# Kernel optimization log

Measured on AMD Instinct MI355X. Metric: run time of the kernel, lower is better.

The kernel has to match this reference:

```python
import jax, jax.numpy as jnp
import numpy as np
import math

B, L, D, H = 2, 2048, 1024, 16
DH = D // H  # d_head = 64
FACTOR = 5


def setup_inputs() -> dict:
    key = jax.random.key(0)
    ks = jax.random.split(key, 6)
    s = 0.02
    x = jax.random.normal(ks[0], (B, L, D), jnp.float32)
    Wq = jax.random.normal(ks[1], (D, D), jnp.float32) * s
    bq = jnp.zeros((D,), jnp.float32)
    Wkv = jax.random.normal(ks[2], (2 * D, D), jnp.float32) * s
    bkv = jnp.zeros((2 * D,), jnp.float32)
    Wout = jax.random.normal(ks[3], (D, D), jnp.float32) * s
    bout = jnp.zeros((D,), jnp.float32)
    U = min(FACTOR * math.ceil(math.log(L)), L)  # 40
    index_sample = jax.random.randint(ks[4], (L, U), 0, L, dtype=jnp.int32)
    return {"x": x, "Wq": Wq, "bq": bq, "Wkv": Wkv, "bkv": bkv,
            "Wout": Wout, "bout": bout, "index_sample": index_sample,
            "factor": FACTOR}


def reference(x, Wq, bq, Wkv, bkv, Wout, bout, index_sample, factor):
    b, l, d = x.shape
    h, dh = H, DH
    scale = 1.0 / math.sqrt(dh)
    u = min(factor * math.ceil(math.log(l)), l)

    # projections (torch Linear: y = x @ W.T + b)
    Q = (x @ Wq.T + bq).reshape(b, l, h, dh).transpose(0, 2, 1, 3)   # [B,H,L,dh]
    KV = x @ Wkv.T + bkv
    K, V = jnp.split(KV, 2, axis=-1)
    K = K.reshape(b, l, h, dh).transpose(0, 2, 1, 3)                  # [B,H,L,dh]
    V = V.reshape(b, l, h, dh).transpose(0, 2, 1, 3)                  # [B,H,L,dh]

    # sampled QK: per query position l, dot with U sampled keys
    K_s = K[:, :, index_sample, :]                                    # [B,H,L,U,dh]
    QK = jnp.einsum('bhld,bhlud->bhlu', Q, K_s)                       # [B,H,L,U]
    M = QK.max(axis=-1) - QK.mean(axis=-1)                            # sparsity measure
    _, top_idx = jax.lax.top_k(M, u)                                  # [B,H,u]

    # full attention only for the top-u queries
    top_q = jnp.take_along_axis(Q, top_idx[..., None], axis=2)        # [B,H,u,dh]
    scores = jnp.einsum('bhud,bhkd->bhuk', top_q, K) * scale          # [B,H,u,L]
    attn = jax.nn.softmax(scores, axis=-1)
    ctx_update = jnp.einsum('bhuk,bhkd->bhud', attn, V)               # [B,H,u,dh]

    # mean-initialized context, scatter updates at top queries
    context = jnp.broadcast_to(V.mean(axis=2, keepdims=True), (b, h, l, dh))
    bI = jnp.arange(b)[:, None, None]
    hI = jnp.arange(h)[None, :, None]
    context = context.at[bI, hI, top_idx].set(ctx_update)             # [B,H,L,dh]

    context = context.transpose(0, 2, 1, 3).reshape(b, l, d)
    return context @ Wout.T + bout
```

## Files before the change

kernel.cpp:

```cpp
#include <hip/hip_runtime.h>
#include <math.h>

#define B_ 2
#define L_ 2048
#define D_ 1024
#define H_ 16
#define DH_ 64
#define U_ 40
#define SCALE_ 0.125f

typedef __attribute__((ext_vector_type(8))) short short8v;
typedef __attribute__((ext_vector_type(4))) float f32x4;
typedef __attribute__((ext_vector_type(4))) unsigned short ushort4v;

static __device__ __forceinline__ unsigned short bf16_rne(float f) {
  unsigned int u = __float_as_uint(f);
  u += 0x7fff + ((u >> 16) & 1);
  return (unsigned short)(u >> 16);
}
static __device__ __forceinline__ float bf16_f32(unsigned short h) {
  return __uint_as_float(((unsigned int)h) << 16);
}

static __device__ __forceinline__ void gload16(const unsigned short* src,
                                               unsigned short* lds) {
  __builtin_amdgcn_global_load_lds(
      (const __attribute__((address_space(1))) void*)src,
      (__attribute__((address_space(3))) void*)lds, 16, 0, 0);
}

#define BARRIER                                  \
  do {                                           \
    asm volatile("" ::: "memory");               \
    __builtin_amdgcn_s_barrier();                \
    asm volatile("" ::: "memory");               \
  } while (0)
#define LGKM0                                          \
  do {                                                 \
    asm volatile("s_waitcnt lgkmcnt(0)" ::: "memory"); \
    __builtin_amdgcn_sched_barrier(0);                 \
  } while (0)

__global__ __launch_bounds__(256) void split_all(
    const float* __restrict__ Wq, const float* __restrict__ Wkv,
    const float* __restrict__ X, unsigned short* __restrict__ Whi,
    unsigned short* __restrict__ Wlo, unsigned short* __restrict__ Xhi,
    unsigned short* __restrict__ Xlo, float* __restrict__ vmAcc, int nW) {
  if (blockIdx.x == 0) {
    for (int z = threadIdx.x; z < B_ * D_; z += 256) vmAcc[z] = 0.f;
  }
  int i = blockIdx.x * 256 + threadIdx.x;
  const int nq_q = (D_ * D_) / 4;
  float4 v;
  unsigned short *hi, *lo;
  int off;
  if (i < nW) {
    v = (i < nq_q) ? ((const float4*)Wq)[i] : ((const float4*)Wkv)[i - nq_q];
    hi = Whi; lo = Wlo; off = i;
  } else {
    off = i - nW;
    v = ((const float4*)X)[off];
    hi = Xhi; lo = Xlo;
  }
  float vv[4] = {v.x, v.y, v.z, v.w};
  ushort4v h, l;
#pragma unroll
  for (int e = 0; e < 4; ++e) {
    unsigned short hh = bf16_rne(vv[e]);
    h[e] = hh;
    l[e] = bf16_rne(vv[e] - bf16_f32(hh));
  }
  ((ushort4v*)hi)[off] = h;
  ((ushort4v*)lo)[off] = l;
}

__global__ __launch_bounds__(512, 1) void gemm_qkv_pipe(
    const unsigned short* __restrict__ Xhi,
    const unsigned short* __restrict__ Xlo,
    const unsigned short* __restrict__ Whi,
    const unsigned short* __restrict__ Wlo,
    const float* __restrict__ bq, const float* __restrict__ bkv,
    float* __restrict__ Qo, float* __restrict__ Ko, float* __restrict__ Vo,
    float* __restrict__ vmAcc) {
  __shared__ unsigned short LDS[3][20480];
  const int tid = threadIdx.x;
  const int lane = tid & 63;
  const int wave = tid >> 6;
  const int wm = wave >> 2, wn = wave & 3;
  const int row0 = blockIdx.y * 128;
  const int col0 = blockIdx.x * 192;

  f32x4 acc[4][3] = {};

  const unsigned short* gsrc[5];
#pragma unroll
  for (int r = 0; r < 5; ++r) {
    int c = wave + 8 * r;
    const unsigned short* base;
    int rowin, isA;
    if (c < 8)       { base = Xhi; rowin = c * 16;        isA = 1; }
    else if (c < 16) { base = Xlo; rowin = (c - 8) * 16;  isA = 1; }
    else if (c < 28) { base = Whi; rowin = (c - 16) * 16; isA = 0; }
    else             { base = Wlo; rowin = (c - 28) * 16; isA = 0; }
    rowin += (lane >> 2);
    int grow = (isA ? row0 : col0) + rowin;
    int seg = (lane & 3) ^ ((rowin >> 1) & 3);
    gsrc[r] = base + (size_t)grow * D_ + seg * 8;
  }

  const int fr_r = lane & 15;
  const int hs = lane >> 4;

#define STG(r, k0s, Ls) \
  gload16(gsrc[r] + (k0s), (Ls) + (wave + 8 * (r)) * 512)

  {
    unsigned short* L0 = &LDS[0][0];
    unsigned short* L1 = &LDS[1][0];
    STG(0, 0, L0); STG(1, 0, L0); STG(2, 0, L0); STG(3, 0, L0); STG(4, 0, L0);
    STG(0, 32, L1); STG(1, 32, L1); STG(2, 32, L1); STG(3, 32, L1);
    STG(4, 32, L1);
  }
  asm volatile("s_waitcnt vmcnt(5)" ::: "memory");
  BARRIER;

  for (int ks = 0; ks < 32; ++ks) {
    unsigned short* Lc = &LDS[ks % 3][0];
    unsigned short* Ls = &LDS[(ks + 2) % 3][0];
    int k0s = (ks + 2) * 32;

    if (ks < 30) {
      STG(0, k0s, Ls); STG(1, k0s, Ls); STG(2, k0s, Ls); STG(3, k0s, Ls);
      STG(4, k0s, Ls);
    }

    short8v a_h[4], a_l[4], b_h[3], b_l[3];
#pragma unroll
    for (int mi = 0; mi < 4; ++mi) {
      int rr = wm * 64 + mi * 16 + fr_r;
      int off = rr * 32 + ((hs ^ ((rr >> 1) & 3)) << 3);
      a_h[mi] = *(const short8v*)&Lc[off];
      a_l[mi] = *(const short8v*)&Lc[4096 + off];
    }
#pragma unroll
    for (int ni = 0; ni < 3; ++ni) {
      int rc = wn * 48 + ni * 16 + fr_r;
      int off = rc * 32 + ((hs ^ ((rc >> 1) & 3)) << 3);
      b_h[ni] = *(const short8v*)&Lc[8192 + off];
      b_l[ni] = *(const short8v*)&Lc[14336 + off];
    }

#pragma unroll
    for (int mi = 0; mi < 4; ++mi)
#pragma unroll
      for (int ni = 0; ni < 3; ++ni) {
        acc[mi][ni] = __builtin_amdgcn_mfma_f32_16x16x32_bf16(
            a_h[mi], b_h[ni], acc[mi][ni], 0, 0, 0);
        acc[mi][ni] = __builtin_amdgcn_mfma_f32_16x16x32_bf16(
            a_h[mi], b_l[ni], acc[mi][ni], 0, 0, 0);
        acc[mi][ni] = __builtin_amdgcn_mfma_f32_16x16x32_bf16(
            a_l[mi], b_h[ni], acc[mi][ni], 0, 0, 0);
      }

    LGKM0;
    if (ks < 30) {
      asm volatile("s_waitcnt vmcnt(5)" ::: "memory");
    } else {
      asm volatile("s_waitcnt vmcnt(0)" ::: "memory");
    }
    BARRIER;
  }

#pragma unroll
  for (int ni = 0; ni < 3; ++ni) {
    int c = col0 + wn * 48 + ni * 16 + (lane & 15);
    int which = c >> 10;
    int jj = c & (D_ - 1);
    int h = jj >> 6, dh = jj & 63;
    float bias = (c < D_) ? bq[c] : bkv[c - D_];
    float* dst = (which == 0) ? Qo : ((which == 1) ? Ko : Vo);
#pragma unroll
    for (int mi = 0; mi < 4; ++mi) {
#pragma unroll
      for (int reg = 0; reg < 4; ++reg) {
        int r = row0 + wm * 64 + mi * 16 + ((lane >> 4) << 2) + reg;
        int b = r >> 11, l = r & (L_ - 1);
        dst[(((size_t)b * H_ + h) * L_ + l) * DH_ + dh] =
            acc[mi][ni][reg] + bias;
      }
    }
    if (which == 2) {
      float s = 0.f;
#pragma unroll
      for (int mi = 0; mi < 4; ++mi)
#pragma unroll
        for (int reg = 0; reg < 4; ++reg) s += acc[mi][ni][reg];
      s += __shfl_xor(s, 16);
      s += __shfl_xor(s, 32);
      if ((lane >> 4) == 0)
        atomicAdd(&vmAcc[(row0 >> 11) * D_ + jj], s + 64.0f * bias);
    }
  }
#undef STG
}

__global__ __launch_bounds__(256) void gemm_qkv_fallback(
    const float* __restrict__ X,
    const unsigned short* __restrict__ Whi,
    const unsigned short* __restrict__ Wlo,
    const float* __restrict__ bq, const float* __restrict__ bkv,
    float* __restrict__ Qo, float* __restrict__ Ko, float* __restrict__ Vo,
    float* __restrict__ vmAcc) {
  __shared__ unsigned short Ah[128 * 32];
  __shared__ unsigned short Al[128 * 32];
  __shared__ unsigned short Bh[128 * 32];
  __shared__ unsigned short Bl[128 * 32];
  const int tid = threadIdx.x;
  const int lane = tid & 63;
  const int wave = tid >> 6;
  const int wm = wave >> 1, wn = wave & 1;
  const int row0 = blockIdx.y * 128;
  const int col0 = blockIdx.x * 128;

  f32x4 acc[4][4] = {};

  const int grow = lane >> 2;
  const int gg = lane & 3;

  for (int k0 = 0; k0 < D_; k0 += 32) {
#pragma unroll
    for (int j = 0; j < 2; ++j) {
      int c = wave + 4 * j;
      int row = c * 16 + grow;
      int gsrc = (gg ^ ((row >> 1) & 3)) << 3;
      size_t soffB = (size_t)(col0 + row) * D_ + k0 + gsrc;
      gload16(Whi + soffB, Bh + c * 512);
      gload16(Wlo + soffB, Bl + c * 512);
    }
#pragma unroll
    for (int rep = 0; rep < 2; ++rep) {
      int task = tid + rep * 256;
      int row = task >> 2;
      int gt = task & 3;
      const float* s = X + (size_t)(row0 + row) * D_ + k0 + gt * 8;
      float4 a0 = *(const float4*)s;
      float4 a1 = *(const float4*)(s + 4);
      float av[8] = {a0.x, a0.y, a0.z, a0.w, a1.x, a1.y, a1.z, a1.w};
      short8v hseg, lseg;
#pragma unroll
      for (int e = 0; e < 8; ++e) {
        unsigned short hh = bf16_rne(av[e]);
        hseg[e] = (short)hh;
        lseg[e] = (short)bf16_rne(av[e] - bf16_f32(hh));
      }
      int dst = row * 32 + ((gt ^ ((row >> 1) & 3)) << 3);
      *(short8v*)&Ah[dst] = hseg;
      *(short8v*)&Al[dst] = lseg;
    }
    __syncthreads();

    short8v a_h[4], a_l[4], b_h[4], b_l[4];
    const int hs = lane >> 4;
#pragma unroll
    for (int mi = 0; mi < 4; ++mi) {
      int rr = wm * 64 + mi * 16 + (lane & 15);
      int off = rr * 32 + ((hs ^ ((rr >> 1) & 3)) << 3);
      a_h[mi] = *(const short8v*)&Ah[off];
      a_l[mi] = *(const short8v*)&Al[off];
    }
#pragma unroll
    for (int ni = 0; ni < 4; ++ni) {
      int rc = wn * 64 + ni * 16 + (lane & 15);
      int off = rc * 32 + ((hs ^ ((rc >> 1) & 3)) << 3);
      b_h[ni] = *(const short8v*)&Bh[off];
      b_l[ni] = *(const short8v*)&Bl[off];
    }
#pragma unroll
    for (int mi = 0; mi < 4; ++mi)
#pragma unroll
      for (int ni = 0; ni < 4; ++ni) {
        acc[mi][ni] = __builtin_amdgcn_mfma_f32_16x16x32_bf16(
            a_h[mi], b_h[ni], acc[mi][ni], 0, 0, 0);
        acc[mi][ni] = __builtin_amdgcn_mfma_f32_16x16x32_bf16(
            a_h[mi], b_l[ni], acc[mi][ni], 0, 0, 0);
        acc[mi][ni] = __builtin_amdgcn_mfma_f32_16x16x32_bf16(
            a_l[mi], b_h[ni], acc[mi][ni], 0, 0, 0);
      }
    __syncthreads();
  }

#pragma unroll
  for (int ni = 0; ni < 4; ++ni) {
    int c = col0 + wn * 64 + ni * 16 + (lane & 15);
    int which = c >> 10;
    int jj = c & (D_ - 1);
    int h = jj >> 6, dh = jj & 63;
    float bias = (c < D_) ? bq[c] : bkv[c - D_];
    float* dst = (which == 0) ? Qo : ((which == 1) ? Ko : Vo);
#pragma unroll
    for (int mi = 0; mi < 4; ++mi) {
#pragma unroll
      for (int reg = 0; reg < 4; ++reg) {
        int r = row0 + wm * 64 + mi * 16 + ((lane >> 4) << 2) + reg;
        int b = r >> 11, l = r & (L_ - 1);
        dst[(((size_t)b * H_ + h) * L_ + l) * DH_ + dh] =
            acc[mi][ni][reg] + bias;
      }
    }
    if (which == 2) {
      float s = 0.f;
#pragma unroll
      for (int mi = 0; mi < 4; ++mi)
#pragma unroll
        for (int reg = 0; reg < 4; ++reg) s += acc[mi][ni][reg];
      s += __shfl_xor(s, 16);
      s += __shfl_xor(s, 32);
      if ((lane >> 4) == 0)
        atomicAdd(&vmAcc[(row0 >> 11) * D_ + jj], s + 64.0f * bias);
    }
  }
}

__global__ __launch_bounds__(256) void sample_base(
    const float* __restrict__ Q, const float* __restrict__ Kt,
    const int* __restrict__ idx, float* __restrict__ Mv,
    const float* __restrict__ vmAcc, const float* __restrict__ Wout,
    const float* __restrict__ bout, float* __restrict__ baseOut,
    float* __restrict__ vmeanM) {
  int t = threadIdx.x;
  if (blockIdx.x < 4096) {
    int w = t >> 6, lane = t & 63;
    int subl = lane >> 4, d16 = lane & 15;
    int gl = blockIdx.x * 16 + w * 4 + subl;
    int bh = gl >> 11, l = gl & (L_ - 1);
    const float4* Kb4 = (const float4*)(Kt + (size_t)bh * L_ * DH_);
    float4 q4 = ((const float4*)(Q + (size_t)gl * DH_))[d16];
    const int* irow = idx + l * U_;
    float mx = -INFINITY, sm = 0.f;
#pragma unroll 8
    for (int u = 0; u < U_; ++u) {
      int kl = irow[u];
      float4 k4 = Kb4[kl * 16 + d16];
      float p = q4.x * k4.x + q4.y * k4.y + q4.z * k4.z + q4.w * k4.w;
      p += __shfl_xor(p, 1);
      p += __shfl_xor(p, 2);
      p += __shfl_xor(p, 4);
      p += __shfl_xor(p, 8);
      mx = fmaxf(mx, p);
      sm += p;
    }
    if (d16 == 0) Mv[gl] = mx - sm * (1.0f / U_);
  } else {
    int bid = blockIdx.x - 4096;
    int b = bid >> 4, jc = bid & 15;
    int j = jc * 64 + (t & 63);
    int isl = t >> 6;
    __shared__ float vm[D_];
    __shared__ float red[256];
    for (int i = t; i < D_; i += 256) vm[i] = vmAcc[b * D_ + i] * (1.0f / L_);
    __syncthreads();
    if (jc == 0)
      for (int i = t; i < D_; i += 256) vmeanM[b * D_ + i] = vm[i];
    float s = 0.f;
    const float* wr = Wout + (size_t)j * D_ + isl * 256;
    const float* vv = vm + isl * 256;
    for (int i = 0; i < 256; i += 4) {
      float4 w = *(const float4*)(wr + i);
      s += vv[i] * w.x + vv[i + 1] * w.y + vv[i + 2] * w.z + vv[i + 3] * w.w;
    }
    red[t] = s;
    __syncthreads();
    if (isl == 0)
      baseOut[b * D_ + j] =
          red[t] + red[t + 64] + red[t + 128] + red[t + 192] + bout[j];
  }
}

__global__ __launch_bounds__(256) void bcast_topk(
    const float* __restrict__ baseIn, float* __restrict__ out,
    const float* __restrict__ Mv, int* __restrict__ topIdx) {
  int t = threadIdx.x;
  if (blockIdx.x < 4096) {
    size_t i4 = (size_t)blockIdx.x * 256 + t;
    size_t i = i4 * 4;
    int b = (int)(i >> 21);
    int col = (int)(i & (D_ - 1));
    *(float4*)(out + i) = *(const float4*)(baseIn + b * D_ + col);
  } else {
    __shared__ float vals[L_];
    int lane = t & 63;
    int bh = blockIdx.x - 4096;
    for (int j = t; j < L_; j += 256) vals[j] = Mv[(size_t)bh * L_ + j];
    __syncthreads();
    for (int it = 0; it < U_; ++it) {
      float bv = -INFINITY;
      int bi = 0x7fffffff;
      for (int j = 0; j < 32; ++j) {
        int i = j * 64 + lane;
        float v = vals[i];
        if (v > bv) { bv = v; bi = i; }
      }
#pragma unroll
      for (int off = 32; off > 0; off >>= 1) {
        float ov = __shfl_xor(bv, off);
        int oi = __shfl_xor(bi, off);
        if (ov > bv || (ov == bv && oi < bi)) { bv = ov; bi = oi; }
      }
      if (t == 0) topIdx[bh * U_ + it] = bi;
      vals[bi] = -INFINITY;
      __syncthreads();
    }
  }
}

__global__ __launch_bounds__(256) void attn_corr(
    const float* __restrict__ Q, const float* __restrict__ Kt,
    const float* __restrict__ Vt, const int* __restrict__ topIdx,
    const float* __restrict__ vmeanM, const float* __restrict__ Wout,
    float* __restrict__ out) {
  int qc = blockIdx.x;
  int bh = blockIdx.y;
  int b = bh >> 4, h = bh & (H_ - 1);
  __shared__ float Qs[5][DH_];
  __shared__ float Sv[5][L_];
  __shared__ float part[4][5][DH_];
  __shared__ float inv[5];
  __shared__ float dv[5][DH_];
  __shared__ int lq[5];
  int t = threadIdx.x;
  int lane = t & 63, w = t >> 6;

  if (t < 80) {
    int q = t >> 4, c4 = t & 15;
    int ql = topIdx[bh * U_ + qc * 5 + q];
    *(float4*)&Qs[q][c4 * 4] =
        *(const float4*)&Q[((size_t)bh * L_ + ql) * DH_ + c4 * 4];
  }
  if (t < 5) lq[t] = topIdx[bh * U_ + qc * 5 + t];
  __syncthreads();

  const float* Kb = Kt + (size_t)bh * L_ * DH_;
  for (int kc = 0; kc < 8; ++kc) {
    int key = kc * 256 + t;
    const float* kr = Kb + (size_t)key * DH_;
    float acc[5];
#pragma unroll
    for (int q = 0; q < 5; ++q) acc[q] = 0.f;
#pragma unroll
    for (int i4 = 0; i4 < 16; ++i4) {
      float4 k4 = *(const float4*)(kr + i4 * 4);
#pragma unroll
      for (int q = 0; q < 5; ++q) {
        float4 qv = *(const float4*)&Qs[q][i4 * 4];
        acc[q] += k4.x * qv.x + k4.y * qv.y + k4.z * qv.z + k4.w * qv.w;
      }
    }
#pragma unroll
    for (int q = 0; q < 5; ++q) Sv[q][key] = acc[q] * SCALE_;
  }
  __syncthreads();

#pragma unroll
  for (int rep = 0; rep < 2; ++rep) {
    int r = (rep == 0) ? w : (w == 0 ? 4 : -1);
    if (r >= 0) {
      float mx = -INFINITY;
      for (int j = 0; j < 32; ++j) mx = fmaxf(mx, Sv[r][j * 64 + lane]);
#pragma unroll
      for (int off = 1; off < 64; off <<= 1)
        mx = fmaxf(mx, __shfl_xor(mx, off));
      float sm = 0.f;
      for (int j = 0; j < 32; ++j) {
        float e = __expf(Sv[r][j * 64 + lane] - mx);
        Sv[r][j * 64 + lane] = e;
        sm += e;
      }
#pragma unroll
      for (int off = 1; off < 64; off <<= 1) sm += __shfl_xor(sm, off);
      if (lane == 0) inv[r] = 1.0f / sm;
    }
  }
  __syncthreads();

  {
    const float* vb = Vt + ((size_t)bh * L_ + w * 512) * DH_ + lane;
    float acc[5];
#pragma unroll
    for (int q = 0; q < 5; ++q) acc[q] = 0.f;
    for (int k4 = 0; k4 < 128; ++k4) {
      float v0 = vb[(k4 * 4 + 0) * DH_];
      float v1 = vb[(k4 * 4 + 1) * DH_];
      float v2 = vb[(k4 * 4 + 2) * DH_];
      float v3 = vb[(k4 * 4 + 3) * DH_];
      int k = w * 512 + k4 * 4;
#pragma unroll
      for (int q = 0; q < 5; ++q) {
        float4 p4 = *(const float4*)&Sv[q][k];
        acc[q] += p4.x * v0 + p4.y * v1 + p4.z * v2 + p4.w * v3;
      }
    }
#pragma unroll
    for (int q = 0; q < 5; ++q) part[w][q][lane] = acc[q];
  }
  __syncthreads();

  for (int o = t; o < 5 * DH_; o += 256) {
    int q = o >> 6, dh = o & 63;
    float s = (part[0][q][dh] + part[1][q][dh]) +
              (part[2][q][dh] + part[3][q][dh]);
    dv[q][dh] = s * inv[q] - vmeanM[b * D_ + h * DH_ + dh];
  }
  __syncthreads();

  int sub = t & 3;
  int jbase = t >> 2;
#pragma unroll
  for (int jc = 0; jc < 16; ++jc) {
    int j = jc * 64 + jbase;
    const float* wr = Wout + (size_t)j * D_ + h * DH_ + sub * 16;
    float4 w0 = ((const float4*)wr)[0];
    float4 w1 = ((const float4*)wr)[1];
    float4 w2 = ((const float4*)wr)[2];
    float4 w3 = ((const float4*)wr)[3];
#pragma unroll
    for (int q = 0; q < 5; ++q) {
      const float* dq = &dv[q][sub * 16];
      float s = dq[0] * w0.x + dq[1] * w0.y + dq[2] * w0.z + dq[3] * w0.w +
                dq[4] * w1.x + dq[5] * w1.y + dq[6] * w1.z + dq[7] * w1.w +
                dq[8] * w2.x + dq[9] * w2.y + dq[10] * w2.z + dq[11] * w2.w +
                dq[12] * w3.x + dq[13] * w3.y + dq[14] * w3.z + dq[15] * w3.w;
      s += __shfl_xor(s, 1);
      s += __shfl_xor(s, 2);
      if (sub == 0)
        atomicAdd(out + ((size_t)b * L_ + lq[q]) * D_ + j, s);
    }
  }
}

extern "C" void kernel_launch(void* const* d_in, const int* in_sizes, int n_in,
                              void* d_out, int out_size, void* d_ws,
                              size_t ws_size, hipStream_t stream) {
  const float* x    = (const float*)d_in[0];
  const float* Wq   = (const float*)d_in[1];
  const float* bq   = (const float*)d_in[2];
  const float* Wkv  = (const float*)d_in[3];
  const float* bkv  = (const float*)d_in[4];
  const float* Wout = (const float*)d_in[5];
  const float* bout = (const float*)d_in[6];
  const int*   idx  = (const int*)d_in[7];
  float* out = (float*)d_out;

  float* ws = (float*)d_ws;
  const size_t NQ = (size_t)B_ * H_ * L_ * DH_;
  float* Q  = ws;
  float* Kt = Q + NQ;
  float* Vt = Kt + NQ;
  unsigned short* Whi = (unsigned short*)(Vt + NQ);
  unsigned short* Wlo = Whi + (size_t)3 * D_ * D_;
  unsigned short* Xhi = Wlo + (size_t)3 * D_ * D_;
  unsigned short* Xlo = Xhi + NQ;
  float* Mv     = Vt + NQ;
  float* vmeanM = Mv + (size_t)B_ * H_ * L_;
  float* baseB  = vmeanM + B_ * D_;
  int*   topIdx = (int*)(baseB + B_ * D_);
  float* vmAcc = out;

  const bool xsplit = ws_size >= ((size_t)76 << 20);
  const int nW = 3 * D_ * D_ / 4;
  const int nX = (int)(NQ / 4);

  if (xsplit) {
    split_all<<<dim3((nW + nX) / 256), dim3(256), 0, stream>>>(
        Wq, Wkv, x, Whi, Wlo, Xhi, Xlo, vmAcc, nW);
    gemm_qkv_pipe<<<dim3(3 * D_ / 192, B_ * L_ / 128), dim3(512), 0,
                    stream>>>(Xhi, Xlo, Whi, Wlo, bq, bkv, Q, Kt, Vt, vmAcc);
  } else {
    split_all<<<dim3(nW / 256), dim3(256), 0, stream>>>(Wq, Wkv, x, Whi, Wlo,
                                                        Xhi, Xlo, vmAcc, nW);
    gemm_qkv_fallback<<<dim3(3 * D_ / 128, B_ * L_ / 128), dim3(256), 0,
                        stream>>>(x, Whi, Wlo, bq, bkv, Q, Kt, Vt, vmAcc);
  }
  sample_base<<<dim3(4096 + B_ * 16), dim3(256), 0, stream>>>(
      Q, Kt, idx, Mv, vmAcc, Wout, bout, baseB, vmeanM);
  bcast_topk<<<dim3(4096 + B_ * H_), dim3(256), 0, stream>>>(baseB, out, Mv,
                                                             topIdx);
  attn_corr<<<dim3(8, 32), dim3(256), 0, stream>>>(Q, Kt, Vt, topIdx, vmeanM,
                                                   Wout, out);
}
```

Before: 238.6 us.

## Enlarge QKV GEMM row tile to 256 with double-buffered LDS

The split-bf16 QKV projection GEMM tile grows from 128x192 to 256x192 per block, so each wave computes 8x3 MFMA tiles and B fragments are reused across twice as many rows. The LDS pipeline drops from three stages to two, and the loop now waits on vmcnt(0) every iteration. The aim is to cut global and LDS traffic per flop. In exchange the grid halves to 16x16=256 blocks, register pressure rises, and load latency is hidden less well.

Result: faster. 229.4 us (-3.9%).

```diff
diff --git a/kernel.cpp b/kernel.cpp
--- a/kernel.cpp
+++ b/kernel.cpp
@@ -74,7 +74,7 @@
   ((ushort4v*)lo)[off] = l;
 }
 
-__global__ __launch_bounds__(512, 1) void gemm_qkv_pipe(
+__global__ __launch_bounds__(512, 1) void gemm_qkv_256(
     const unsigned short* __restrict__ Xhi,
     const unsigned short* __restrict__ Xlo,
     const unsigned short* __restrict__ Whi,
@@ -82,26 +82,26 @@
     const float* __restrict__ bq, const float* __restrict__ bkv,
     float* __restrict__ Qo, float* __restrict__ Ko, float* __restrict__ Vo,
     float* __restrict__ vmAcc) {
-  __shared__ unsigned short LDS[3][20480];
+  __shared__ unsigned short LDS[2][28672];
   const int tid = threadIdx.x;
   const int lane = tid & 63;
   const int wave = tid >> 6;
   const int wm = wave >> 2, wn = wave & 3;
-  const int row0 = blockIdx.y * 128;
+  const int row0 = blockIdx.y * 256;
   const int col0 = blockIdx.x * 192;
 
-  f32x4 acc[4][3] = {};
-
-  const unsigned short* gsrc[5];
-#pragma unroll
-  for (int r = 0; r < 5; ++r) {
+  f32x4 acc[8][3] = {};
+
+  const unsigned short* gsrc[7];
+#pragma unroll
+  for (int r = 0; r < 7; ++r) {
     int c = wave + 8 * r;
     const unsigned short* base;
     int rowin, isA;
-    if (c < 8)       { base = Xhi; rowin = c * 16;        isA = 1; }
-    else if (c < 16) { base = Xlo; rowin = (c - 8) * 16;  isA = 1; }
-    else if (c < 28) { base = Whi; rowin = (c - 16) * 16; isA = 0; }
-    else             { base = Wlo; rowin = (c - 28) * 16; isA = 0; }
+    if (c < 16)      { base = Xhi; rowin = c * 16;        isA = 1; }
+    else if (c < 32) { base = Xlo; rowin = (c - 16) * 16; isA = 1; }
+    else if (c < 44) { base = Whi; rowin = (c - 32) * 16; isA = 0; }
+    else             { base = Wlo; rowin = (c - 44) * 16; isA = 0; }
     rowin += (lane >> 2);
     int grow = (isA ? row0 : col0) + rowin;
     int seg = (lane & 3) ^ ((rowin >> 1) & 3);
@@ -112,62 +112,53 @@
   const int hs = lane >> 4;
 
 #define STG(r, k0s, Ls) \
-  gload16(gsrc[r] + (k0s), (Ls) + (wave + 8 * (r)) * 512)
+  gload16(gsrc[r] + (k0s), (Ls) + ((wave + 8 * (r)) * 512))
 
   {
     unsigned short* L0 = &LDS[0][0];
-    unsigned short* L1 = &LDS[1][0];
-    STG(0, 0, L0); STG(1, 0, L0); STG(2, 0, L0); STG(3, 0, L0); STG(4, 0, L0);
-    STG(0, 32, L1); STG(1, 32, L1); STG(2, 32, L1); STG(3, 32, L1);
-    STG(4, 32, L1);
-  }
-  asm volatile("s_waitcnt vmcnt(5)" ::: "memory");
+    STG(0, 0, L0); STG(1, 0, L0); STG(2, 0, L0); STG(3, 0, L0);
+    STG(4, 0, L0); STG(5, 0, L0); STG(6, 0, L0);
+  }
+  asm volatile("s_waitcnt vmcnt(0)" ::: "memory");
   BARRIER;
 
   for (int ks = 0; ks < 32; ++ks) {
-    unsigned short* Lc = &LDS[ks % 3][0];
-    unsigned short* Ls = &LDS[(ks + 2) % 3][0];
-    int k0s = (ks + 2) * 32;
-
-    if (ks < 30) {
+    unsigned short* Lc = &LDS[ks & 1][0];
+    unsigned short* Ls = &LDS[(ks + 1) & 1][0];
+    int k0s = (ks + 1) * 32;
+
+    if (ks < 31) {
       STG(0, k0s, Ls); STG(1, k0s, Ls); STG(2, k0s, Ls); STG(3, k0s, Ls);
-      STG(4, k0s, Ls);
-    }
-
-    short8v a_h[4], a_l[4], b_h[3], b_l[3];
-#pragma unroll
-    for (int mi = 0; mi < 4; ++mi) {
-      int rr = wm * 64 + mi * 16 + fr_r;
-      int off = rr * 32 + ((hs ^ ((rr >> 1) & 3)) << 3);
-      a_h[mi] = *(const short8v*)&Lc[off];
-      a_l[mi] = *(const short8v*)&Lc[4096 + off];
-    }
+      STG(4, k0s, Ls); STG(5, k0s, Ls); STG(6, k0s, Ls);
+    }
+
+    short8v b_h[3], b_l[3];
 #pragma unroll
     for (int ni = 0; ni < 3; ++ni) {
       int rc = wn * 48 + ni * 16 + fr_r;
       int off = rc * 32 + ((hs ^ ((rc >> 1) & 3)) << 3);
-      b_h[ni] = *(const short8v*)&Lc[8192 + off];
-      b_l[ni] = *(const short8v*)&Lc[14336 + off];
-    }
-
-#pragma unroll
-    for (int mi = 0; mi < 4; ++mi)
+      b_h[ni] = *(const short8v*)&Lc[16384 + off];
+      b_l[ni] = *(const short8v*)&Lc[22528 + off];
+    }
+#pragma unroll
+    for (int mi = 0; mi < 8; ++mi) {
+      int rr = wm * 128 + mi * 16 + fr_r;
+      int off = rr * 32 + ((hs ^ ((rr >> 1) & 3)) << 3);
+      short8v a_h = *(const short8v*)&Lc[off];
+      short8v a_l = *(const short8v*)&Lc[8192 + off];
 #pragma unroll
       for (int ni = 0; ni < 3; ++ni) {
         acc[mi][ni] = __builtin_amdgcn_mfma_f32_16x16x32_bf16(
-            a_h[mi], b_h[ni], acc[mi][ni], 0, 0, 0);
+            a_h, b_h[ni], acc[mi][ni], 0, 0, 0);
         acc[mi][ni] = __builtin_amdgcn_mfma_f32_16x16x32_bf16(
-            a_h[mi], b_l[ni], acc[mi][ni], 0, 0, 0);
+            a_h, b_l[ni], acc[mi][ni], 0, 0, 0);
         acc[mi][ni] = __builtin_amdgcn_mfma_f32_16x16x32_bf16(
-            a_l[mi], b_h[ni], acc[mi][ni], 0, 0, 0);
-      }
+            a_l, b_h[ni], acc[mi][ni], 0, 0, 0);
+      }
+    }
 
     LGKM0;
-    if (ks < 30) {
-      asm volatile("s_waitcnt vmcnt(5)" ::: "memory");
-    } else {
-      asm volatile("s_waitcnt vmcnt(0)" ::: "memory");
-    }
+    asm volatile("s_waitcnt vmcnt(0)" ::: "memory");
     BARRIER;
   }
 
@@ -180,10 +171,10 @@
     float bias = (c < D_) ? bq[c] : bkv[c - D_];
     float* dst = (which == 0) ? Qo : ((which == 1) ? Ko : Vo);
 #pragma unroll
-    for (int mi = 0; mi < 4; ++mi) {
+    for (int mi = 0; mi < 8; ++mi) {
 #pragma unroll
       for (int reg = 0; reg < 4; ++reg) {
-        int r = row0 + wm * 64 + mi * 16 + ((lane >> 4) << 2) + reg;
+        int r = row0 + wm * 128 + mi * 16 + ((lane >> 4) << 2) + reg;
         int b = r >> 11, l = r & (L_ - 1);
         dst[(((size_t)b * H_ + h) * L_ + l) * DH_ + dh] =
             acc[mi][ni][reg] + bias;
@@ -192,13 +183,13 @@
     if (which == 2) {
       float s = 0.f;
 #pragma unroll
-      for (int mi = 0; mi < 4; ++mi)
+      for (int mi = 0; mi < 8; ++mi)
 #pragma unroll
         for (int reg = 0; reg < 4; ++reg) s += acc[mi][ni][reg];
       s += __shfl_xor(s, 16);
       s += __shfl_xor(s, 32);
       if ((lane >> 4) == 0)
-        atomicAdd(&vmAcc[(row0 >> 11) * D_ + jj], s + 64.0f * bias);
+        atomicAdd(&vmAcc[(row0 >> 11) * D_ + jj], s + 128.0f * bias);
     }
   }
 #undef STG
@@ -572,8 +563,8 @@
   if (xsplit) {
     split_all<<<dim3((nW + nX) / 256), dim3(256), 0, stream>>>(
         Wq, Wkv, x, Whi, Wlo, Xhi, Xlo, vmAcc, nW);
-    gemm_qkv_pipe<<<dim3(3 * D_ / 192, B_ * L_ / 128), dim3(512), 0,
-                    stream>>>(Xhi, Xlo, Whi, Wlo, bq, bkv, Q, Kt, Vt, vmAcc);
+    gemm_qkv_256<<<dim3(3 * D_ / 192, B_ * L_ / 256), dim3(512), 0,
+                   stream>>>(Xhi, Xlo, Whi, Wlo, bq, bkv, Q, Kt, Vt, vmAcc);
   } else {
     split_all<<<dim3(nW / 256), dim3(256), 0, stream>>>(Wq, Wkv, x, Whi, Wlo,
                                                         Xhi, Xlo, vmAcc, nW);
```
